# Kernel optimization log

Measured on AMD Instinct MI355X. Metric: run time of the kernel, lower is better.

The kernel has to match this reference:

```python
import jax, jax.numpy as jnp
import numpy as np

EPS = 1e-8
EPS12 = 1e-12
TAU = 0.2
IOU_THRESHOLD = 0.5
NEG_INF = -1e9

N, C = 8192, 1024
HID, FGD, CLSD = 256, 64, 128


def setup_inputs() -> dict:
    key = jax.random.key(0)
    ks = jax.random.split(key, 16)
    roi_feats = jax.random.normal(ks[0], (N, C), dtype=jnp.float32)
    # labels in {-1 (ignore), 0 (bg), 1..20 (classes)}
    labels = jax.random.randint(ks[1], (N,), 0, 21, dtype=jnp.int64) - 1
    ious = jax.random.uniform(ks[2], (N,), dtype=jnp.float32)
    s = 0.02
    w1f = jax.random.normal(ks[3], (HID, C), dtype=jnp.float32) * s
    b1f = jnp.zeros((HID,), dtype=jnp.float32)
    w2f = jax.random.normal(ks[4], (FGD, HID), dtype=jnp.float32) * s
    b2f = jnp.zeros((FGD,), dtype=jnp.float32)
    w1c = jax.random.normal(ks[5], (HID, C), dtype=jnp.float32) * s
    b1c = jnp.zeros((HID,), dtype=jnp.float32)
    w2c = jax.random.normal(ks[6], (CLSD, HID), dtype=jnp.float32) * s
    b2c = jnp.zeros((CLSD,), dtype=jnp.float32)
    return {"roi_feats": roi_feats, "labels": labels, "ious": ious,
            "w1f": w1f, "b1f": b1f, "w2f": w2f, "b2f": b2f,
            "w1c": w1c, "b1c": b1c, "w2c": w2c, "b2c": b2c}


def _project_normalize(x, w1, b1, w2, b2):
    h = jax.nn.relu(x @ w1.T + b1)
    z = h @ w2.T + b2
    nrm = jnp.linalg.norm(z, axis=1, keepdims=True)  # F.normalize: z / max(||z||, eps)
    return z / jnp.maximum(nrm, EPS)


def _fg_bg_loss(z_fg, fg_mask, ignore_mask, iou_weight):
    n = z_fg.shape[0]
    anchor = fg_mask & ~ignore_mask
    eye = jnp.eye(n, dtype=bool)
    # pos_mask[i,j] = fg_mask[j] & ~ignore[j], self excluded
    pos = (fg_mask & ~ignore_mask)[None, :] & ~eye  # [N,N]
    sim = (z_fg @ z_fg.T) / TAU
    sim_exp = jnp.exp(sim) * (~eye).astype(sim.dtype)
    denom = sim_exp.sum(axis=1)  # [N]
    numer = jnp.sum(jnp.exp(sim) * pos.astype(sim.dtype), axis=1)  # [N]
    n_pos = pos.sum(axis=1)
    loss_i = -jnp.log((numer + EPS) / (denom + EPS))
    valid = anchor & (n_pos > 0)
    w = iou_weight
    num = jnp.sum(jnp.where(valid, loss_i * w, 0.0))
    den = jnp.sum(jnp.where(valid, w, 0.0)) + EPS
    return num / den


def _class_supcon_loss(z_cls, labels, fg_mask, ignore_mask, iou_weight):
    n = z_cls.shape[0]
    anchor = fg_mask & ~ignore_mask
    eye = jnp.eye(n, dtype=bool)
    valid_den = ~eye & ~ignore_mask[None, :]  # [N,N]
    # pos[i,j]: same label, j not ignored, labels[j] != 0, j != i, j valid
    pos = (labels[None, :] == labels[:, None]) & ~ignore_mask[None, :] & (labels[None, :] != 0)
    pos = pos & ~eye & valid_den
    sim = (z_cls @ z_cls.T) / TAU
    logits = jnp.where(valid_den, sim, NEG_INF)
    denom_log = jax.nn.logsumexp(logits, axis=1)  # [N]
    n_pos = pos.sum(axis=1)
    sum_pos = jnp.sum(jnp.where(pos, sim, 0.0), axis=1)
    n_pos_safe = jnp.maximum(n_pos, 1).astype(sim.dtype)
    loss_i = -(sum_pos - n_pos.astype(sim.dtype) * denom_log) / n_pos_safe
    valid = anchor & (n_pos > 0) & valid_den.any(axis=1)
    w = iou_weight
    num = jnp.sum(jnp.where(valid, loss_i * w, 0.0))
    den = jnp.sum(jnp.where(valid, w, 0.0)) + EPS12
    return num / den


def reference(roi_feats, labels, ious, w1f, b1f, w2f, b2f, w1c, b1c, w2c, b2c):
    z_fg = _project_normalize(roi_feats, w1f, b1f, w2f, b2f)
    z_cls = _project_normalize(roi_feats, w1c, b1c, w2c, b2c)
    ignore_mask = labels == -1
    bg_mask = (labels == 0) & ~ignore_mask
    fg_mask = (labels > 0) & ~ignore_mask
    iou_weight = jnp.where(ious > IOU_THRESHOLD, ious, 0.0)
    loss_fg_bg = _fg_bg_loss(z_fg, fg_mask, ignore_mask, iou_weight)
    loss_supcon = _class_supcon_loss(z_cls, labels, fg_mask, ignore_mask, iou_weight)
    # loss_weights = (1.0, 1.0); stacked as [loss_fg_bg, loss_supcon]
    return jnp.stack([loss_fg_bg * 1.0, loss_supcon * 1.0])
```

## Files before the change

### kernel.cpp

```cpp
#include <hip/hip_runtime.h>
#include <hip/hip_bf16.h>
#include <math.h>

#define N_ROI 8192
#define C_IN  1024
#define HIDD  256
#define FGD   64
#define CLSD  128
#define INV_TAU 5.0f
#define SCALE_LOG2E 7.2134752f
#define LN2F 0.69314718f

using frag_ab = __attribute__((ext_vector_type(8))) short;
using f32x16  = __attribute__((ext_vector_type(16))) float;

static __device__ __forceinline__ short f32_to_bf16_bits(float f) {
  unsigned u = __builtin_bit_cast(unsigned, f);
  u = (u + 0x7FFFu + ((u >> 16) & 1u)) >> 16;
  return (short)u;
}
static __device__ __forceinline__ float bf16_bits_to_f32(short b) {
  unsigned u = ((unsigned)(unsigned short)b) << 16;
  return __builtin_bit_cast(float, u);
}
static __device__ __forceinline__ float fast_exp2(float x) {
#if __has_builtin(__builtin_amdgcn_exp2f)
  return __builtin_amdgcn_exp2f(x);
#else
  return exp2f(x);
#endif
}

__global__ __launch_bounds__(256) void pack_zero_kernel(
    const float* __restrict__ w1f, const float* __restrict__ w1c,
    const float* __restrict__ w2f, const float* __restrict__ w2c,
    short* __restrict__ W1pf, short* __restrict__ W1pc,
    short* __restrict__ W2pf, short* __restrict__ W2pc,
    float* __restrict__ accum, int* __restrict__ cnt) {
  int b = blockIdx.x;
  if (b == 280) {
    int t = threadIdx.x;
    if (t < 8) accum[t] = 0.f;
    if (t < 24) cnt[t] = 0;
    return;
  }
  const float* src; short* dst; int Ksh; int b0;
  if (b < 128)      { src = w1f; dst = W1pf; Ksh = 10; b0 = 0; }
  else if (b < 256) { src = w1c; dst = W1pc; Ksh = 10; b0 = 128; }
  else if (b < 264) { src = w2f; dst = W2pf; Ksh = 8;  b0 = 256; }
  else              { src = w2c; dst = W2pc; Ksh = 8;  b0 = 264; }
  int K = 1 << Ksh;
  int f = (b - b0) * 256 + threadIdx.x;
  int r = f >> (Ksh - 3);
  int c0 = (f & ((K >> 3) - 1)) << 3;
  float4 v0 = *(const float4*)(src + (size_t)r * K + c0);
  float4 v1 = *(const float4*)(src + (size_t)r * K + c0 + 4);
  union { short s[8]; uint4 v; } o;
  o.s[0] = f32_to_bf16_bits(v0.x); o.s[1] = f32_to_bf16_bits(v0.y);
  o.s[2] = f32_to_bf16_bits(v0.z); o.s[3] = f32_to_bf16_bits(v0.w);
  o.s[4] = f32_to_bf16_bits(v1.x); o.s[5] = f32_to_bf16_bits(v1.y);
  o.s[6] = f32_to_bf16_bits(v1.z); o.s[7] = f32_to_bf16_bits(v1.w);
  ((uint4*)dst)[(size_t)((r >> 5) * (K >> 4) + (c0 >> 4)) * 64 +
                ((c0 >> 3) & 1) * 32 + (r & 31)] = o.v;
}

template<int D>
__device__ __forceinline__ void gemm2_from_lds(
    const short* __restrict__ T2,
    const short* __restrict__ W2p, const float* __restrict__ b2,
    short* __restrict__ Zr, float* __restrict__ tii,
    short* __restrict__ T, int gt) {
  int lane = threadIdx.x & 63;
  const frag_ab* Wv = (const frag_ab*)W2p;
  constexpr int NT = D / 32;
  frag_ab a[16];
  #pragma unroll
  for (int kc = 0; kc < 16; ++kc)
    a[kc] = *(const frag_ab*)&T2[(lane & 31) * 264 + kc * 16 + (lane >> 5) * 8];
  f32x16 acc[NT];
  #pragma unroll
  for (int j = 0; j < NT; ++j)
    #pragma unroll
    for (int q = 0; q < 16; ++q) acc[j][q] = 0.f;
  #pragma unroll
  for (int kc = 0; kc < 16; ++kc)
    #pragma unroll
    for (int j = 0; j < NT; ++j)
      acc[j] = __builtin_amdgcn_mfma_f32_32x32x16_bf16(a[kc], Wv[(j * 16 + kc) * 64 + lane], acc[j], 0, 0, 0);
  int c = lane & 31, h = lane >> 5;
  float bb[NT];
  #pragma unroll
  for (int j = 0; j < NT; ++j) bb[j] = b2[j * 32 + c];
  float s1[16];
  #pragma unroll
  for (int r = 0; r < 16; ++r) {
    s1[r] = 0.f;
    #pragma unroll
    for (int j = 0; j < NT; ++j) {
      float v = acc[j][r] + bb[j];
      s1[r] += v * v;
    }
  }
  #pragma unroll
  for (int r = 0; r < 16; ++r)
    #pragma unroll
    for (int m = 1; m < 32; m <<= 1) s1[r] += __shfl_xor(s1[r], m);
  float s2[16];
  #pragma unroll
  for (int r = 0; r < 16; ++r) s2[r] = 0.f;
  #pragma unroll
  for (int j = 0; j < NT; ++j) {
    int cl = j * 32 + c;
    #pragma unroll
    for (int g = 0; g < 4; ++g) {
      short q0, q1, q2, q3;
      #pragma unroll
      for (int e = 0; e < 4; ++e) {
        int r = g * 4 + e;
        float sc = 1.f / fmaxf(sqrtf(s1[r]), 1e-8f);
        short qb = f32_to_bf16_bits((acc[j][r] + bb[j]) * sc);
        float zf = bf16_bits_to_f32(qb);
        s2[r] += zf * zf;
        if (e == 0) q0 = qb; else if (e == 1) q1 = qb; else if (e == 2) q2 = qb; else q3 = qb;
      }
      *(short4*)&T[cl * 36 + 4 * h + 8 * g] = make_short4(q0, q1, q2, q3);
    }
  }
  #pragma unroll
  for (int r = 0; r < 16; ++r)
    #pragma unroll
    for (int m = 1; m < 32; m <<= 1) s2[r] += __shfl_xor(s2[r], m);
  if (c == 0) {
    #pragma unroll
    for (int r = 0; r < 16; ++r)
      tii[gt * 32 + (r & 3) + 8 * (r >> 2) + 4 * h] = s2[r];
  }
  uint4* Zv = (uint4*)Zr;
  #pragma unroll
  for (int k = 0; k < D / 16; ++k) {
    int c0 = (2 * k + h) * 8;
    union { short s[8]; uint4 u; } o;
    #pragma unroll
    for (int e = 0; e < 8; ++e) o.s[e] = T[(c0 + e) * 36 + c];
    Zv[(size_t)(gt * (D / 16) + k) * 64 + h * 32 + c] = o.u;
  }
}

__global__ __launch_bounds__(256) void fused_mlp_kernel(
    const float* __restrict__ X,
    const short* __restrict__ W1pf, const short* __restrict__ W1pc,
    const float* __restrict__ b1f, const float* __restrict__ b1c,
    const short* __restrict__ W2pf, const short* __restrict__ W2pc,
    const float* __restrict__ b2f, const float* __restrict__ b2c,
    short* __restrict__ Zrf, short* __restrict__ Zrc,
    float* __restrict__ tiif, float* __restrict__ tiic,
    const int* __restrict__ labels,
    float* __restrict__ Sfg, float* __restrict__ Pfg,
    float* __restrict__ Scls, float* __restrict__ SPc,
    float* __restrict__ pfv, float* __restrict__ nimv,
    float* __restrict__ ljmv, int* __restrict__ cnt) {
  __shared__ short stageA[2][1024];
  __shared__ short T2[32 * 264];
  __shared__ short Tw[128 * 36];
  int tid = threadIdx.x, lane = tid & 63, wv = tid >> 6;
  int Mb = blockIdx.x, head = blockIdx.y;

  if (head == 0 && tid < 32) {
    int i = Mb * 32 + tid;
    Sfg[i] = 0.f; Pfg[i] = 0.f; Scls[i] = 0.f; SPc[i] = 0.f;
    int l = labels[i];
    pfv[i]  = (l > 0)  ? 1.f : 0.f;
    nimv[i] = (l != -1) ? 1.f : 0.f;
    ljmv[i] = (l > 0)  ? (float)l : -7.f;
    int b = l + 1; if (b < 0) b = 0; if (b > 21) b = 21;
    atomicAdd(&cnt[b], 1);
  }

  const short* Wp = head ? W1pc : W1pf;
  const float* b1 = head ? b1c  : b1f;
  const uint4* Wv4 = (const uint4*)Wp;
  int arow = tid >> 3;
  int ac4  = tid & 7;
  const float* Xp = X + (size_t)(Mb * 32 + arow) * C_IN + ac4 * 4;
  int aslot = ((ac4 >> 2) * 64 + ((ac4 >> 1) & 1) * 32 + arow) * 8 + (ac4 & 1) * 4;

  float4 av;
  frag_ab breg[2][4];
  f32x16 acc[2];
  #pragma unroll
  for (int nt = 0; nt < 2; ++nt)
    #pragma unroll
    for (int q = 0; q < 16; ++q) acc[nt][q] = 0.f;

  auto loadA = [&](int c) { av = *(const float4*)(Xp + c * 32); };
  auto loadB = [&](int c, int s) {
    #pragma unroll
    for (int kci = 0; kci < 2; ++kci)
      #pragma unroll
      for (int nt = 0; nt < 2; ++nt)
        breg[s][kci * 2 + nt] =
            *(const frag_ab*)&Wv4[(size_t)((wv * 2 + nt) * 64 + c * 2 + kci) * 64 + lane];
  };
  auto storeA = [&](int buf) {
    *(short4*)&stageA[buf][aslot] =
        make_short4(f32_to_bf16_bits(av.x), f32_to_bf16_bits(av.y),
                    f32_to_bf16_bits(av.z), f32_to_bf16_bits(av.w));
  };
  auto domfma = [&](int buf, int bank) {
    frag_ab a0 = *(const frag_ab*)&stageA[buf][(0 * 64 + lane) * 8];
    frag_ab a1 = *(const frag_ab*)&stageA[buf][(1 * 64 + lane) * 8];
    #pragma unroll
    for (int nt = 0; nt < 2; ++nt)
      acc[nt] = __builtin_amdgcn_mfma_f32_32x32x16_bf16(a0, breg[bank][nt], acc[nt], 0, 0, 0);
    #pragma unroll
    for (int nt = 0; nt < 2; ++nt)
      acc[nt] = __builtin_amdgcn_mfma_f32_32x32x16_bf16(a1, breg[bank][2 + nt], acc[nt], 0, 0, 0);
  };

  loadA(0); loadB(0, 0); storeA(0);
  __syncthreads();
  for (int c = 0; c < 32; c += 2) {
    if (c + 1 < 32) { loadA(c + 1); loadB(c + 1, 1); }
    domfma(0, 0);
    if (c + 1 < 32) storeA(1);
    __syncthreads();
    if (c + 2 < 32) { loadA(c + 2); loadB(c + 2, 0); }
    domfma(1, 1);
    if (c + 2 < 32) storeA(0);
    __syncthreads();
  }
  {
    int cl31 = lane & 31, h = lane >> 5;
    #pragma unroll
    for (int nt = 0; nt < 2; ++nt) {
      int gc = wv * 64 + nt * 32 + cl31;
      float bb = b1[gc];
      #pragma unroll
      for (int q = 0; q < 16; ++q) {
        int row = (q & 3) + 8 * (q >> 2) + 4 * h;
        float x = fmaxf(acc[nt][q] + bb, 0.f);
        T2[row * 264 + gc] = f32_to_bf16_bits(x);
      }
    }
  }
  __syncthreads();

  if (wv == 0) {
    if (head == 0)
      gemm2_from_lds<FGD>(T2, W2pf, b2f, Zrf, tiif, Tw, Mb);
    else
      gemm2_from_lds<CLSD>(T2, W2pc, b2c, Zrc, tiic, Tw, Mb);
  }
}

template<int D, int MODE, int NJT>
__device__ __forceinline__ void loss_body(
    const short* __restrict__ Zr, const int* __restrict__ labels,
    const float* __restrict__ pfv, const float* __restrict__ nimv,
    const float* __restrict__ ljmv,
    float* __restrict__ Sg, float* __restrict__ Pg) {
  constexpr int KC = D / 16;
  int tid = threadIdx.x, lane = tid & 63, wv = tid >> 6;
  int itile = blockIdx.x * 4 + wv;
  const frag_ab* Zrv = (const frag_ab*)Zr;
  frag_ab a[KC];
  #pragma unroll
  for (int kc = 0; kc < KC; ++kc) {
    frag_ab t = Zrv[(itile * KC + kc) * 64 + lane];
    #pragma unroll
    for (int e = 0; e < 8; ++e)
      t[e] = f32_to_bf16_bits(bf16_bits_to_f32(t[e]) * SCALE_LOG2E);
    a[kc] = t;
  }
  float limf[16];
  if (MODE == 1) {
    #pragma unroll
    for (int r = 0; r < 16; ++r) {
      int row = (r & 3) + 8 * (r >> 2) + 4 * (lane >> 5);
      limf[r] = (float)labels[itile * 32 + row];
    }
  }
  float Ssum[16] = {}, Psum[16] = {};
  int jt0 = blockIdx.y * NJT;
  int jlane = lane & 31;

  #pragma unroll 2
  for (int kk = 0; kk < NJT; ++kk) {
    int jt = jt0 + kk;
    int j = jt * 32 + jlane;
    float pf = 0.f, nim = 0.f, ljm = 0.f;
    if (MODE == 0) pf = pfv[j];
    else { nim = nimv[j]; ljm = ljmv[j]; }
    f32x16 acc;
    #pragma unroll
    for (int q = 0; q < 16; ++q) acc[q] = 0.f;
    #pragma unroll
    for (int kc = 0; kc < KC; ++kc) {
      frag_ab b = Zrv[((size_t)jt * KC + kc) * 64 + lane];
      acc = __builtin_amdgcn_mfma_f32_32x32x16_bf16(a[kc], b, acc, 0, 0, 0);
    }
    #pragma unroll
    for (int rr = 0; rr < 16; ++rr) {
      float e = fast_exp2(acc[rr]);
      if (MODE == 0) {
        Ssum[rr] += e;
        Psum[rr] = fmaf(pf, e, Psum[rr]);
      } else {
        Ssum[rr] = fmaf(nim, e, Ssum[rr]);
        Psum[rr] += (limf[rr] == ljm) ? acc[rr] : 0.f;
      }
    }
  }
  #pragma unroll
  for (int r = 0; r < 16; ++r) {
    float s = Ssum[r], p = Psum[r];
    #pragma unroll
    for (int m = 1; m < 32; m <<= 1) { s += __shfl_xor(s, m); p += __shfl_xor(p, m); }
    if ((lane & 31) == 0) {
      if (MODE == 1) p *= LN2F;
      int row = (r & 3) + 8 * (r >> 2) + 4 * (lane >> 5);
      atomicAdd(&Sg[itile * 32 + row], s);
      atomicAdd(&Pg[itile * 32 + row], p);
    }
  }
}

__global__ __launch_bounds__(256, 4) void loss_kernel(
    const short* __restrict__ Zrf, const short* __restrict__ Zrc,
    const int* __restrict__ labels,
    const float* __restrict__ pfv, const float* __restrict__ nimv,
    const float* __restrict__ ljmv,
    float* __restrict__ Sfg, float* __restrict__ Pfg,
    float* __restrict__ Scls, float* __restrict__ SPc) {
  if (blockIdx.z == 0)
    loss_body<FGD, 0, 16>(Zrf, labels, pfv, nimv, ljmv, Sfg, Pfg);
  else
    loss_body<CLSD, 1, 16>(Zrc, labels, pfv, nimv, ljmv, Scls, SPc);
}

__global__ __launch_bounds__(256) void finalize_kernel(
    const float* __restrict__ Sfg, const float* __restrict__ Pfg,
    const float* __restrict__ Scls, const float* __restrict__ SPc,
    const float* __restrict__ tiif, const float* __restrict__ tiic,
    const int* __restrict__ labels, const float* __restrict__ ious,
    int* __restrict__ cnt, float* __restrict__ accum, float* __restrict__ out) {
  int i = blockIdx.x * 256 + threadIdx.x;
  int l = labels[i];
  float iv = ious[i];
  float w = (iv > 0.5f) ? iv : 0.f;
  int cntP = 0;
  #pragma unroll
  for (int b = 2; b <= 21; ++b) cntP += cnt[b];
  int cntNI = N_ROI - cnt[0];
  bool Pi = (l > 0);
  float numF = 0.f, denF = 0.f, numC = 0.f, denC = 0.f;
  float eF = __expf(INV_TAU * tiif[i]);
  float Sf = Sfg[i] - eF;
  float Pf = Pfg[i] - (Pi ? eF : 0.f);
  int nposF = cntP - (Pi ? 1 : 0);
  if (Pi && nposF > 0) {
    float lossF = logf((Sf + 1e-8f) / (Pf + 1e-8f));
    numF = lossF * w; denF = w;
  }
  float tC = INV_TAU * tiic[i];
  float eC = __expf(tC);
  float Sc = Scls[i] - ((l != -1) ? eC : 0.f);
  float SP = SPc[i] - (Pi ? tC : 0.f);
  int nposC = Pi ? (cnt[l + 1] - 1) : 0;
  bool anyv = (cntNI - ((l != -1) ? 1 : 0)) > 0;
  if (Pi && nposC > 0 && anyv) {
    float lse = logf(Sc);
    float lossC = -(SP - (float)nposC * lse) / fmaxf((float)nposC, 1.f);
    numC = lossC * w; denC = w;
  }
  float v0 = numF, v1 = denF, v2 = numC, v3 = denC;
  #pragma unroll
  for (int m = 1; m < 64; m <<= 1) {
    v0 += __shfl_xor(v0, m); v1 += __shfl_xor(v1, m);
    v2 += __shfl_xor(v2, m); v3 += __shfl_xor(v3, m);
  }
  __shared__ float red[4][4];
  int lane = threadIdx.x & 63, wid = threadIdx.x >> 6;
  if (lane == 0) { red[wid][0]=v0; red[wid][1]=v1; red[wid][2]=v2; red[wid][3]=v3; }
  __syncthreads();
  if (threadIdx.x == 0) {
    float s0=0,s1=0,s2=0,s3=0;
    for (int q = 0; q < 4; ++q) { s0+=red[q][0]; s1+=red[q][1]; s2+=red[q][2]; s3+=red[q][3]; }
    atomicAdd(&accum[0], s0); atomicAdd(&accum[1], s1);
    atomicAdd(&accum[2], s2); atomicAdd(&accum[3], s3);
    __threadfence();
    int t = atomicAdd(&cnt[22], 1);
    if (t == 31) {
      __threadfence();
      out[0] = accum[0] / (accum[1] + 1e-8f);
      out[1] = accum[2] / (accum[3] + 1e-12f);
    }
  }
}

extern "C" void kernel_launch(void* const* d_in, const int* in_sizes, int n_in,
                              void* d_out, int out_size, void* d_ws, size_t ws_size,
                              hipStream_t stream) {
  const float* X    = (const float*)d_in[0];
  const int*  labels= (const int*)d_in[1];
  const float* ious = (const float*)d_in[2];
  const float* w1f  = (const float*)d_in[3];
  const float* b1f  = (const float*)d_in[4];
  const float* w2f  = (const float*)d_in[5];
  const float* b2f  = (const float*)d_in[6];
  const float* w1c  = (const float*)d_in[7];
  const float* b1c  = (const float*)d_in[8];
  const float* w2c  = (const float*)d_in[9];
  const float* b2c  = (const float*)d_in[10];
  float* out = (float*)d_out;

  char* w = (char*)d_ws;
  short* W1pf = (short*)w;            w += 524288;
  short* W1pc = (short*)w;            w += 524288;
  short* W2pf = (short*)w;            w += 32768;
  short* W2pc = (short*)w;            w += 65536;
  short* Zrf  = (short*)w;            w += 1048576;
  short* Zrc  = (short*)w;            w += 2097152;
  float* Sfg  = (float*)w;            w += 32768;
  float* Pfg  = (float*)w;            w += 32768;
  float* Scls = (float*)w;            w += 32768;
  float* SPc  = (float*)w;            w += 32768;
  float* tiif = (float*)w;            w += 32768;
  float* tiic = (float*)w;            w += 32768;
  float* pfv  = (float*)w;            w += 32768;
  float* nimv = (float*)w;            w += 32768;
  float* ljmv = (float*)w;            w += 32768;
  float* accum= (float*)w;            w += 32;
  int*   cnt  = (int*)w;              w += 96;

  pack_zero_kernel<<<281, 256, 0, stream>>>(w1f, w1c, w2f, w2c,
                                            W1pf, W1pc, W2pf, W2pc, accum, cnt);

  fused_mlp_kernel<<<dim3(256, 2), 256, 0, stream>>>(X, W1pf, W1pc, b1f, b1c,
                                            W2pf, W2pc, b2f, b2c,
                                            Zrf, Zrc, tiif, tiic,
                                            labels, Sfg, Pfg, Scls, SPc,
                                            pfv, nimv, ljmv, cnt);

  loss_kernel<<<dim3(64, 16, 2), 256, 0, stream>>>(Zrf, Zrc, labels, pfv, nimv, ljmv,
                                                   Sfg, Pfg, Scls, SPc);

  finalize_kernel<<<N_ROI/256, 256, 0, stream>>>(Sfg, Pfg, Scls, SPc, tiif, tiic,
                                                 labels, ious, cnt, accum, out);
}
```

Measured before the change: 197.7 us.

## Double-buffer j-tiles in LDS via async global-to-LDS loads in loss kernel

The loss kernel now stages each j-tile of normalized embeddings into a double-buffered LDS region using global_load_lds async copies, shared by the block's four waves instead of each wave loading B fragments from global memory. The next tile's copy is issued before the current MFMA and exp work, and a waitcnt plus barrier at each iteration end swaps the buffers. It also interleaves fg and cls blocks along blockIdx.x in place of a z dimension, and raises wave priority around the MFMA loop. The per-iteration barrier and vmcnt(0) wait can serialize the waves and reduce latency hiding, and unroll 2 is dropped.

```diff
diff --git a/kernel.cpp b/kernel.cpp
--- a/kernel.cpp
+++ b/kernel.cpp
@@ -29,6 +29,11 @@
 #else
   return exp2f(x);
 #endif
+}
+static __device__ __forceinline__ void async_copy16(const short* g, short* l) {
+  __builtin_amdgcn_global_load_lds(
+      (const __attribute__((address_space(1))) unsigned int*)g,
+      (__attribute__((address_space(3))) unsigned int*)l, 16, 0, 0);
 }
 
 __global__ __launch_bounds__(256) void pack_zero_kernel(
@@ -258,10 +263,13 @@
     const short* __restrict__ Zr, const int* __restrict__ labels,
     const float* __restrict__ pfv, const float* __restrict__ nimv,
     const float* __restrict__ ljmv,
-    float* __restrict__ Sg, float* __restrict__ Pg) {
+    float* __restrict__ Sg, float* __restrict__ Pg,
+    short* __restrict__ jbuf) {
   constexpr int KC = D / 16;
+  constexpr int TSH = KC * 64 * 8;
+  constexpr int LD = (KC * 64) / 256;
   int tid = threadIdx.x, lane = tid & 63, wv = tid >> 6;
-  int itile = blockIdx.x * 4 + wv;
+  int itile = (blockIdx.x >> 1) * 4 + wv;
   const frag_ab* Zrv = (const frag_ab*)Zr;
   frag_ab a[KC];
   #pragma unroll
@@ -284,21 +292,35 @@
   int jt0 = blockIdx.y * NJT;
   int jlane = lane & 31;
 
-  #pragma unroll 2
+  auto STAGE = [&](short* dst, int kk) {
+    const short* src = Zr + (size_t)(jt0 + kk) * KC * 512;
+    #pragma unroll
+    for (int u = 0; u < LD; ++u)
+      async_copy16(src + (size_t)(u * 256 + tid) * 8,
+                   dst + (u * 256 + (wv * 64)) * 8);
+  };
+
+  STAGE(jbuf, 0);
+  asm volatile("s_waitcnt vmcnt(0)" ::: "memory");
+  __builtin_amdgcn_s_barrier();
+  short* cur = jbuf; short* nxt = jbuf + TSH;
+
   for (int kk = 0; kk < NJT; ++kk) {
-    int jt = jt0 + kk;
-    int j = jt * 32 + jlane;
+    if (kk + 1 < NJT) STAGE(nxt, kk + 1);
+    int j = (jt0 + kk) * 32 + jlane;
     float pf = 0.f, nim = 0.f, ljm = 0.f;
     if (MODE == 0) pf = pfv[j];
     else { nim = nimv[j]; ljm = ljmv[j]; }
     f32x16 acc;
     #pragma unroll
     for (int q = 0; q < 16; ++q) acc[q] = 0.f;
+    __builtin_amdgcn_s_setprio(1);
     #pragma unroll
     for (int kc = 0; kc < KC; ++kc) {
-      frag_ab b = Zrv[((size_t)jt * KC + kc) * 64 + lane];
+      frag_ab b = *(const frag_ab*)&cur[(kc * 64 + lane) * 8];
       acc = __builtin_amdgcn_mfma_f32_32x32x16_bf16(a[kc], b, acc, 0, 0, 0);
     }
+    __builtin_amdgcn_s_setprio(0);
     #pragma unroll
     for (int rr = 0; rr < 16; ++rr) {
       float e = fast_exp2(acc[rr]);
@@ -310,7 +332,11 @@
         Psum[rr] += (limf[rr] == ljm) ? acc[rr] : 0.f;
       }
     }
-  }
+    asm volatile("s_waitcnt vmcnt(0)" ::: "memory");
+    __builtin_amdgcn_s_barrier();
+    short* t = cur; cur = nxt; nxt = t;
+  }
+
   #pragma unroll
   for (int r = 0; r < 16; ++r) {
     float s = Ssum[r], p = Psum[r];
@@ -332,10 +358,11 @@
     const float* __restrict__ ljmv,
     float* __restrict__ Sfg, float* __restrict__ Pfg,
     float* __restrict__ Scls, float* __restrict__ SPc) {
-  if (blockIdx.z == 0)
-    loss_body<FGD, 0, 16>(Zrf, labels, pfv, nimv, ljmv, Sfg, Pfg);
+  __shared__ short jbuf[2 * 8 * 64 * 8];
+  if ((blockIdx.x & 1) == 0)
+    loss_body<FGD, 0, 16>(Zrf, labels, pfv, nimv, ljmv, Sfg, Pfg, jbuf);
   else
-    loss_body<CLSD, 1, 16>(Zrc, labels, pfv, nimv, ljmv, Scls, SPc);
+    loss_body<CLSD, 1, 16>(Zrc, labels, pfv, nimv, ljmv, Scls, SPc, jbuf);
 }
 
 __global__ __launch_bounds__(256) void finalize_kernel(
@@ -442,8 +469,8 @@
                                             labels, Sfg, Pfg, Scls, SPc,
                                             pfv, nimv, ljmv, cnt);
 
-  loss_kernel<<<dim3(64, 16, 2), 256, 0, stream>>>(Zrf, Zrc, labels, pfv, nimv, ljmv,
-                                                   Sfg, Pfg, Scls, SPc);
+  loss_kernel<<<dim3(128, 16), 256, 0, stream>>>(Zrf, Zrc, labels, pfv, nimv, ljmv,
+                                                 Sfg, Pfg, Scls, SPc);
 
   finalize_kernel<<<N_ROI/256, 256, 0, stream>>>(Sfg, Pfg, Scls, SPc, tiif, tiic,
                                                  labels, ious, cnt, accum, out);
```

Result: faster. 188.2 us (-4.8%).
